# Optimization experiments

Measured on AMD Instinct MI355X. Metric: run time of the kernel, lower is better.

The kernel has to match this reference:

```python
import jax, jax.numpy as jnp
import numpy as np

N_NODES = 100000


def _mean_agg(x, src, dst, n_nodes):
    # gather neighbor (src) features, segment-sum into destination nodes, divide by in-degree
    summed = jax.ops.segment_sum(x[src], dst, num_segments=n_nodes)  # [N, d]
    deg = jax.ops.segment_sum(jnp.ones_like(dst, dtype=x.dtype), dst, num_segments=n_nodes)
    return summed / jnp.clip(deg, 1.0)[:, None]  # DGL clamps zero in-degree to 1


def _sage_conv(x, src, dst, W_self, W_neigh, b, n_nodes):
    h_neigh = _mean_agg(x, src, dst, n_nodes)
    # DGL SAGEConv(mean): fc_self(h_self) + fc_neigh(h_neigh); single bias
    return x @ W_self + h_neigh @ W_neigh + b


def setup_inputs() -> dict:
    key = jax.random.key(0)
    ks = jax.random.split(key, 8)
    in_f, hid_f, out_f = 64, 64, 16
    n_edges = 1200000
    return {
        "x": jax.random.normal(ks[0], (N_NODES, in_f), dtype=jnp.float32),
        "src": jax.random.randint(ks[1], (n_edges,), 0, N_NODES),
        "dst": jax.random.randint(ks[2], (n_edges,), 0, N_NODES),
        "W1_self": jax.random.normal(ks[3], (in_f, hid_f), dtype=jnp.float32) / np.sqrt(in_f),
        "W1_neigh": jax.random.normal(ks[4], (in_f, hid_f), dtype=jnp.float32) / np.sqrt(in_f),
        "b1": jnp.zeros((hid_f,), dtype=jnp.float32),
        "W2_self": jax.random.normal(ks[5], (hid_f, out_f), dtype=jnp.float32) / np.sqrt(hid_f),
        "W2_neigh": jax.random.normal(ks[6], (hid_f, out_f), dtype=jnp.float32) / np.sqrt(hid_f),
        "b2": jnp.zeros((out_f,), dtype=jnp.float32),
    }


def reference(x, src, dst, W1_self, W1_neigh, b1, W2_self, W2_neigh, b2):
    h = _sage_conv(x, src, dst, W1_self, W1_neigh, b1, N_NODES)
    h = jax.nn.relu(h)
    h = _sage_conv(h, src, dst, W2_self, W2_neigh, b2, N_NODES)
    return h
```

## Files before the change

### kernel.cpp

```cpp
#include <hip/hip_runtime.h>

#define N_NODES 100000
#define N_EDGES 1200000
#define BK 64
#define NB 1563
#define CHUNK_E 4096
#define NBLK_E 293
#define TOT_H (NB * NBLK_E)
#define NSB2 ((TOT_H + 1023) / 1024)
#define CAP 1536
#define ND1 3125

#define OFF_ROWPTR 0
#define OFF_HISTG  401408
#define OFF_BLK2   2234368
#define OFF_PAIRS  2236416
#define OFF_SORTED 7036928
#define OFF_Y1     11837440
#define OFF_H1     24637440

__device__ __forceinline__ unsigned short f2bf(float f) {
    unsigned u = __float_as_uint(f);
    unsigned r = (u + 0x7fffu + ((u >> 16) & 1u)) >> 16;
    return (unsigned short)r;
}

__global__ __launch_bounds__(256) void hist_dense1_kernel(
    const int* __restrict__ dst, int* __restrict__ hist_g,
    const float* __restrict__ x,
    const float* __restrict__ Wn, const float* __restrict__ Ws,
    const float* __restrict__ b,
    unsigned short* __restrict__ y1, float* __restrict__ z1)
{
    __shared__ float sx[32 * 64];
    const int t = threadIdx.x;

    if (blockIdx.x < NBLK_E) {
        int* h = (int*)sx;
        const int e0 = blockIdx.x * CHUNK_E;
        const int e1 = min(e0 + CHUNK_E, N_EDGES);
        for (int i = t; i < NB; i += 256) h[i] = 0;
        __syncthreads();
        for (int e = e0 + t; e < e1; e += 256)
            atomicAdd(&h[dst[e] >> 6], 1);
        __syncthreads();
        for (int i = t; i < NB; i += 256)
            hist_g[i * NBLK_E + blockIdx.x] = h[i];
        return;
    }

    const int bid = blockIdx.x - NBLK_E;
    const int w = t >> 6;
    const int lane = t & 63;
    const int half = w >> 1;
    const int nsub = (w & 1) * 16;
    const int chunk = bid * 32;

    {
        const float4* gx = (const float4*)(x + (size_t)chunk * 64);
        float4* sx4 = (float4*)sx;
        sx4[t] = gx[t];
        sx4[t + 256] = gx[t + 256];
    }

    const float* W = half ? Ws : Wn;
    float wr[64];
#pragma unroll
    for (int k = 0; k < 64; ++k) wr[k] = W[k * 64 + lane];
    const float bj = half ? b[lane] : 0.f;

    __syncthreads();

#pragma unroll 2
    for (int m = 0; m < 16; ++m) {
        const int node = nsub + m;
        const float4* xr = (const float4*)(sx + node * 64);
        float a0 = 0.f, a1 = 0.f, a2 = 0.f, a3 = 0.f;
#pragma unroll
        for (int k4 = 0; k4 < 16; ++k4) {
            float4 v = xr[k4];
            a0 += v.x * wr[4 * k4 + 0];
            a1 += v.y * wr[4 * k4 + 1];
            a2 += v.z * wr[4 * k4 + 2];
            a3 += v.w * wr[4 * k4 + 3];
        }
        const float o = (a0 + a1) + (a2 + a3) + bj;
        const size_t gn = (size_t)(chunk + node);
        if (half) z1[gn * 64 + lane] = o;
        else      y1[gn * 64 + lane] = f2bf(o);
    }
}

__global__ __launch_bounds__(1024) void scan2_blocks_kernel(
    int* __restrict__ hist_g, int* __restrict__ blk2)
{
    __shared__ int wsum[16];
    const int t = threadIdx.x;
    const int i = blockIdx.x * 1024 + t;
    const int v = (i < TOT_H) ? hist_g[i] : 0;
    int inc = v;
#pragma unroll
    for (int off = 1; off < 64; off <<= 1) {
        int n = __shfl_up(inc, off);
        if ((t & 63) >= off) inc += n;
    }
    const int wid = t >> 6;
    if ((t & 63) == 63) wsum[wid] = inc;
    __syncthreads();
    if (t < 16) {
        int s = wsum[t];
#pragma unroll
        for (int off = 1; off < 16; off <<= 1) {
            int n = __shfl_up(s, off);
            if (t >= off) s += n;
        }
        wsum[t] = s;
    }
    __syncthreads();
    const int base = (wid > 0) ? wsum[wid - 1] : 0;
    const int incl = inc + base;
    if (i < TOT_H) hist_g[i] = incl - v;
    if (t == 1023) blk2[blockIdx.x] = incl;
}

__global__ __launch_bounds__(512) void tops_scan_kernel(int* __restrict__ blk2)
{
    __shared__ int wsum[8];
    const int t = threadIdx.x;
    const int v = (t < NSB2) ? blk2[t] : 0;
    int inc = v;
#pragma unroll
    for (int off = 1; off < 64; off <<= 1) {
        int n = __shfl_up(inc, off);
        if ((t & 63) >= off) inc += n;
    }
    const int wid = t >> 6;
    if ((t & 63) == 63) wsum[wid] = inc;
    __syncthreads();
    if (t < 8) {
        int s = wsum[t];
#pragma unroll
        for (int off = 1; off < 8; off <<= 1) {
            int n = __shfl_up(s, off);
            if (t >= off) s += n;
        }
        wsum[t] = s;
    }
    __syncthreads();
    const int base = (wid > 0) ? wsum[wid - 1] : 0;
    if (t < NSB2) blk2[t] = inc + base - v;
}

__global__ __launch_bounds__(512) void pair_scatter_kernel(
    const int* __restrict__ src, const int* __restrict__ dst,
    const int* __restrict__ hs_scan, const int* __restrict__ blk2,
    unsigned* __restrict__ pairs)
{
    __shared__ int base_s[NB];
    __shared__ int cur_s[NB];
    const int b = blockIdx.x;
    const int t = threadIdx.x;
    const int e0 = b * CHUNK_E;
    const int e1 = min(e0 + CHUNK_E, N_EDGES);

    for (int i = t; i < NB; i += 512) {
        int idx = i * NBLK_E + b;
        base_s[i] = hs_scan[idx] + blk2[idx >> 10];
        cur_s[i] = 0;
    }
    __syncthreads();
    for (int e = e0 + t; e < e1; e += 512) {
        int d = dst[e];
        int bk = d >> 6;
        int pos = base_s[bk] + atomicAdd(&cur_s[bk], 1);
        pairs[pos] = ((unsigned)src[e] << 6) | (unsigned)(d & 63);
    }
}

__global__ __launch_bounds__(512) void fused_gather1_kernel(
    const unsigned short* __restrict__ y1,
    const unsigned* __restrict__ pairs,
    const int* __restrict__ hs_scan, const int* __restrict__ blk2,
    int* __restrict__ row_ptr, int* __restrict__ sorted_src,
    float* __restrict__ h1)
{
    __shared__ int slist[CAP];
    __shared__ int hist[BK];
    __shared__ int sc[BK];
    __shared__ int cur[BK];
    const int b = blockIdx.x;
    const int t = threadIdx.x;

    const int i0 = b * NBLK_E;
    const int start = hs_scan[i0] + blk2[i0 >> 10];
    const int end = (b == NB - 1) ? N_EDGES
                    : hs_scan[i0 + NBLK_E] + blk2[(i0 + NBLK_E) >> 10];
    const int cnt = end - start;
    const int node0 = b * BK;

    if (t < BK) hist[t] = 0;
    __syncthreads();
    for (int e = start + t; e < end; e += 512)
        atomicAdd(&hist[pairs[e] & 63u], 1);
    __syncthreads();

    int v = 0;
    if (t < BK) {
        v = hist[t];
        int inc = v;
#pragma unroll
        for (int off = 1; off < 64; off <<= 1) {
            int n = __shfl_up(inc, off);
            if (t >= off) inc += n;
        }
        sc[t] = inc;
    }
    __syncthreads();
    const int excl = (t < BK) ? sc[t] - v : 0;
    if (t < BK && node0 + t < N_NODES) row_ptr[node0 + t] = start + excl;
    if (b == NB - 1 && t == 0) row_ptr[N_NODES] = N_EDGES;
    if (t < BK) cur[t] = excl;
    __syncthreads();

    const int wv = t >> 6;
    const int lane = t & 63;
    const int sub = lane >> 5;
    const int sl = lane & 31;
    const int eg = sl >> 3;
    const int fl = sl & 7;

    if (cnt <= CAP) {
        for (int e = start + t; e < end; e += 512) {
            unsigned u = pairs[e];
            int p = atomicAdd(&cur[u & 63u], 1);
            slist[p] = (int)(u >> 6);
        }
        __syncthreads();
        for (int i = t; i < cnt; i += 512)
            sorted_src[start + i] = slist[i];
        for (int q = 0; q < 4; ++q) {
            const int node = wv * 8 + q * 2 + sub;
            const int gn = node0 + node;
            if (gn >= N_NODES) break;
            const int o = sc[node] - hist[node];
            const int dg = hist[node];
            float4* hp = (float4*)(h1 + (size_t)gn * 64);
            float4 z;
            if (eg < 2) z = hp[fl * 2 + eg];
            float a0 = 0.f, a1 = 0.f, a2 = 0.f, a3 = 0.f;
            float a4 = 0.f, a5 = 0.f, a6 = 0.f, a7 = 0.f;
            for (int base = 0; base < dg; base += 8) {
                const int i0e = base + eg;
                const int i1e = base + 4 + eg;
                const bool v0 = i0e < dg, v1 = i1e < dg;
                uint4 r0, r1;
                if (v0) {
                    const int s = slist[o + i0e];
                    r0 = ((const uint4*)(y1 + (size_t)s * 64))[fl];
                }
                if (v1) {
                    const int s = slist[o + i1e];
                    r1 = ((const uint4*)(y1 + (size_t)s * 64))[fl];
                }
                if (v0) {
                    a0 += __uint_as_float(r0.x << 16);
                    a1 += __uint_as_float(r0.x & 0xffff0000u);
                    a2 += __uint_as_float(r0.y << 16);
                    a3 += __uint_as_float(r0.y & 0xffff0000u);
                    a4 += __uint_as_float(r0.z << 16);
                    a5 += __uint_as_float(r0.z & 0xffff0000u);
                    a6 += __uint_as_float(r0.w << 16);
                    a7 += __uint_as_float(r0.w & 0xffff0000u);
                }
                if (v1) {
                    a0 += __uint_as_float(r1.x << 16);
                    a1 += __uint_as_float(r1.x & 0xffff0000u);
                    a2 += __uint_as_float(r1.y << 16);
                    a3 += __uint_as_float(r1.y & 0xffff0000u);
                    a4 += __uint_as_float(r1.z << 16);
                    a5 += __uint_as_float(r1.z & 0xffff0000u);
                    a6 += __uint_as_float(r1.w << 16);
                    a7 += __uint_as_float(r1.w & 0xffff0000u);
                }
            }
#pragma unroll
            for (int d = 8; d <= 16; d <<= 1) {
                a0 += __shfl_xor(a0, d); a1 += __shfl_xor(a1, d);
                a2 += __shfl_xor(a2, d); a3 += __shfl_xor(a3, d);
                a4 += __shfl_xor(a4, d); a5 += __shfl_xor(a5, d);
                a6 += __shfl_xor(a6, d); a7 += __shfl_xor(a7, d);
            }
            const float invd = 1.0f / (float)max(dg, 1);
            if (eg == 0) {
                hp[fl * 2] = make_float4(fmaxf(z.x + a0 * invd, 0.f),
                                         fmaxf(z.y + a1 * invd, 0.f),
                                         fmaxf(z.z + a2 * invd, 0.f),
                                         fmaxf(z.w + a3 * invd, 0.f));
            } else if (eg == 1) {
                hp[fl * 2 + 1] = make_float4(fmaxf(z.x + a4 * invd, 0.f),
                                             fmaxf(z.y + a5 * invd, 0.f),
                                             fmaxf(z.z + a6 * invd, 0.f),
                                             fmaxf(z.w + a7 * invd, 0.f));
            }
        }
    } else {
        if (t < BK) cur[t] = start + excl;
        __syncthreads();
        for (int e = start + t; e < end; e += 512) {
            unsigned u = pairs[e];
            int p = atomicAdd(&cur[u & 63u], 1);
            sorted_src[p] = (int)(u >> 6);
        }
        __syncthreads();
        for (int q = 0; q < 4; ++q) {
            const int node = wv * 8 + q * 2 + sub;
            const int gn = node0 + node;
            if (gn >= N_NODES) break;
            const int o = start + sc[node] - hist[node];
            const int dg = hist[node];
            float4* hp = (float4*)(h1 + (size_t)gn * 64);
            float4 z;
            if (eg < 2) z = hp[fl * 2 + eg];
            float a0 = 0.f, a1 = 0.f, a2 = 0.f, a3 = 0.f;
            float a4 = 0.f, a5 = 0.f, a6 = 0.f, a7 = 0.f;
            for (int base = 0; base < dg; base += 4) {
                const int idx = base + eg;
                if (idx < dg) {
                    const int s = sorted_src[o + idx];
                    uint4 raw = ((const uint4*)(y1 + (size_t)s * 64))[fl];
                    a0 += __uint_as_float(raw.x << 16);
                    a1 += __uint_as_float(raw.x & 0xffff0000u);
                    a2 += __uint_as_float(raw.y << 16);
                    a3 += __uint_as_float(raw.y & 0xffff0000u);
                    a4 += __uint_as_float(raw.z << 16);
                    a5 += __uint_as_float(raw.z & 0xffff0000u);
                    a6 += __uint_as_float(raw.w << 16);
                    a7 += __uint_as_float(raw.w & 0xffff0000u);
                }
            }
#pragma unroll
            for (int d = 8; d <= 16; d <<= 1) {
                a0 += __shfl_xor(a0, d); a1 += __shfl_xor(a1, d);
                a2 += __shfl_xor(a2, d); a3 += __shfl_xor(a3, d);
                a4 += __shfl_xor(a4, d); a5 += __shfl_xor(a5, d);
                a6 += __shfl_xor(a6, d); a7 += __shfl_xor(a7, d);
            }
            const float invd = 1.0f / (float)max(dg, 1);
            if (eg == 0) {
                hp[fl * 2] = make_float4(fmaxf(z.x + a0 * invd, 0.f),
                                         fmaxf(z.y + a1 * invd, 0.f),
                                         fmaxf(z.z + a2 * invd, 0.f),
                                         fmaxf(z.w + a3 * invd, 0.f));
            } else if (eg == 1) {
                hp[fl * 2 + 1] = make_float4(fmaxf(z.x + a4 * invd, 0.f),
                                             fmaxf(z.y + a5 * invd, 0.f),
                                             fmaxf(z.z + a6 * invd, 0.f),
                                             fmaxf(z.w + a7 * invd, 0.f));
            }
        }
    }
}

__global__ __launch_bounds__(256) void dense2_kernel(
    const float* __restrict__ h1,
    const float* __restrict__ Wn, const float* __restrict__ Ws,
    const float* __restrict__ b,
    float* __restrict__ y2, float* __restrict__ out)
{
    __shared__ float sx[32 * 68];
    const int t = threadIdx.x;
    const int w = t >> 6;
    const int lane = t & 63;
    const int half = w >> 1;
    const int nsub = (w & 1) * 16;
    const int j = lane & 15;
    const int g = lane >> 4;
    const int chunk = blockIdx.x * 32;

    {
        const float4* gx = (const float4*)(h1 + (size_t)chunk * 64);
        float4* sx4 = (float4*)sx;
        int r0 = t >> 4, c0 = t & 15;
        sx4[r0 * 17 + c0] = gx[t];
        sx4[(r0 + 16) * 17 + c0] = gx[t + 256];
    }

    const float* W = half ? Ws : Wn;
    float wr[64];
#pragma unroll
    for (int k = 0; k < 64; ++k) wr[k] = W[k * 16 + j];
    const float bj = half ? b[j] : 0.f;

    __syncthreads();

#pragma unroll 2
    for (int q = 0; q < 4; ++q) {
        const int node = nsub + q * 4 + g;
        const float4* xr = (const float4*)(sx + node * 68);
        float a0 = 0.f, a1 = 0.f, a2 = 0.f, a3 = 0.f;
#pragma unroll
        for (int k4 = 0; k4 < 16; ++k4) {
            float4 v = xr[k4];
            a0 += v.x * wr[4 * k4 + 0];
            a1 += v.y * wr[4 * k4 + 1];
            a2 += v.z * wr[4 * k4 + 2];
            a3 += v.w * wr[4 * k4 + 3];
        }
        const float o = (a0 + a1) + (a2 + a3) + bj;
        const size_t gn = (size_t)(chunk + node);
        if (half) out[gn * 16 + j] = o;
        else      y2[gn * 16 + j] = o;
    }
}

__global__ __launch_bounds__(256) void gather2_kernel(
    const float* __restrict__ y2,
    const int* __restrict__ row_ptr,
    const int* __restrict__ sorted_src,
    float* __restrict__ out)
{
    const int wv = threadIdx.x >> 6;
    const int lane = threadIdx.x & 63;
    const int sub = lane >> 4;
    const int sl = lane & 15;
    const int eg = sl >> 2;
    const int fl = sl & 3;

    const int n = blockIdx.x * 16 + wv * 4 + sub;
    const int start = row_ptr[n];
    const int deg = row_ptr[n + 1] - start;

    float4* op = (float4*)(out + (size_t)n * 16);
    float4 z;
    if (eg == 0) z = op[fl];

    float4 acc = make_float4(0.f, 0.f, 0.f, 0.f);
    for (int base = 0; base < deg; base += 16) {
        int eid = 0;
        if (base + sl < deg) eid = sorted_src[start + base + sl];
#pragma unroll
        for (int jj = 0; jj < 16; jj += 4) {
            const int idx = jj + eg;
            const int s = __shfl(eid, sub * 16 + idx);
            if (base + idx < deg) {
                float4 v = ((const float4*)(y2 + (size_t)s * 16))[fl];
                acc.x += v.x; acc.y += v.y; acc.z += v.z; acc.w += v.w;
            }
        }
    }
#pragma unroll
    for (int d = 4; d <= 8; d <<= 1) {
        acc.x += __shfl_xor(acc.x, d); acc.y += __shfl_xor(acc.y, d);
        acc.z += __shfl_xor(acc.z, d); acc.w += __shfl_xor(acc.w, d);
    }
    const float invd = 1.0f / (float)max(deg, 1);
    if (eg == 0) {
        op[fl] = make_float4(z.x + acc.x * invd, z.y + acc.y * invd,
                             z.z + acc.z * invd, z.w + acc.w * invd);
    }
}

extern "C" void kernel_launch(void* const* d_in, const int* in_sizes, int n_in,
                              void* d_out, int out_size, void* d_ws, size_t ws_size,
                              hipStream_t stream) {
    const float* x   = (const float*)d_in[0];
    const int*   src = (const int*)d_in[1];
    const int*   dst = (const int*)d_in[2];
    const float* W1s = (const float*)d_in[3];
    const float* W1n = (const float*)d_in[4];
    const float* b1  = (const float*)d_in[5];
    const float* W2s = (const float*)d_in[6];
    const float* W2n = (const float*)d_in[7];
    const float* b2  = (const float*)d_in[8];
    float* out = (float*)d_out;

    char* ws = (char*)d_ws;
    int* row_ptr    = (int*)(ws + OFF_ROWPTR);
    int* hist_g     = (int*)(ws + OFF_HISTG);
    int* blk2       = (int*)(ws + OFF_BLK2);
    unsigned* pairs = (unsigned*)(ws + OFF_PAIRS);
    int* sorted_src = (int*)(ws + OFF_SORTED);
    unsigned short* y1 = (unsigned short*)(ws + OFF_Y1);
    float* y2       = (float*)(ws + OFF_Y1);
    float* h1       = (float*)(ws + OFF_H1);

    hist_dense1_kernel<<<NBLK_E + ND1, 256, 0, stream>>>(
        dst, hist_g, x, W1n, W1s, b1, y1, h1);
    scan2_blocks_kernel<<<NSB2, 1024, 0, stream>>>(hist_g, blk2);
    tops_scan_kernel<<<1, 512, 0, stream>>>(blk2);
    pair_scatter_kernel<<<NBLK_E, 512, 0, stream>>>(src, dst, hist_g, blk2, pairs);
    fused_gather1_kernel<<<NB, 512, 0, stream>>>(y1, pairs, hist_g, blk2,
                                                 row_ptr, sorted_src, h1);
    dense2_kernel<<<ND1, 256, 0, stream>>>(h1, W2n, W2s, b2, y2, out);
    gather2_kernel<<<N_NODES / 16, 256, 0, stream>>>(y2, row_ptr, sorted_src, out);
}
```

Before: 217.1 us.

## Fuse layer-2 dense projection into layer-1 gather kernel epilogue

The layer-2 projection (h1 times W2_neigh and W2_self plus bias) now runs in the epilogue of the layer-1 gather kernel, using W2 held in shared memory and shuffle reductions, so the separate dense2 kernel is removed. The relu'd h1 row stays in registers instead of being written back and re-read from global memory, and one launch disappears. y2 moves to its own workspace region because y1 is still being read during the fused pass. The cost is more shared memory, more registers and more work per block in the gather kernel, which may lower occupancy.

```diff
diff --git a/kernel.cpp b/kernel.cpp
--- a/kernel.cpp
+++ b/kernel.cpp
@@ -18,6 +18,7 @@
 #define OFF_SORTED 7036928
 #define OFF_Y1     11837440
 #define OFF_H1     24637440
+#define OFF_Y2     50237440
 
 __device__ __forceinline__ unsigned short f2bf(float f) {
     unsigned u = __float_as_uint(f);
@@ -181,15 +182,25 @@
     const unsigned short* __restrict__ y1,
     const unsigned* __restrict__ pairs,
     const int* __restrict__ hs_scan, const int* __restrict__ blk2,
+    const float* __restrict__ h1,
+    const float* __restrict__ W2n, const float* __restrict__ W2s,
+    const float* __restrict__ b2,
     int* __restrict__ row_ptr, int* __restrict__ sorted_src,
-    float* __restrict__ h1)
+    float* __restrict__ y2, float* __restrict__ outp)
 {
     __shared__ int slist[CAP];
     __shared__ int hist[BK];
     __shared__ int sc[BK];
     __shared__ int cur[BK];
+    __shared__ float sW2n[64 * 17];
+    __shared__ float sW2s[64 * 17];
     const int b = blockIdx.x;
     const int t = threadIdx.x;
+
+    for (int e = t; e < 1024; e += 512) {
+        sW2n[(e >> 4) * 17 + (e & 15)] = W2n[e];
+        sW2s[(e >> 4) * 17 + (e & 15)] = W2s[e];
+    }
 
     const int i0 = b * NBLK_E;
     const int start = hs_scan[i0] + blk2[i0 >> 10];
@@ -228,6 +239,7 @@
     const int sl = lane & 31;
     const int eg = sl >> 3;
     const int fl = sl & 7;
+    const float4 bb = ((const float4*)b2)[eg];
 
     if (cnt <= CAP) {
         for (int e = start + t; e < end; e += 512) {
@@ -244,9 +256,9 @@
             if (gn >= N_NODES) break;
             const int o = sc[node] - hist[node];
             const int dg = hist[node];
-            float4* hp = (float4*)(h1 + (size_t)gn * 64);
-            float4 z;
-            if (eg < 2) z = hp[fl * 2 + eg];
+            const float4* hp = (const float4*)(h1 + (size_t)gn * 64);
+            const float4 z0 = hp[fl * 2];
+            const float4 z1v = hp[fl * 2 + 1];
             float a0 = 0.f, a1 = 0.f, a2 = 0.f, a3 = 0.f;
             float a4 = 0.f, a5 = 0.f, a6 = 0.f, a7 = 0.f;
             for (int base = 0; base < dg; base += 8) {
@@ -291,16 +303,41 @@
                 a6 += __shfl_xor(a6, d); a7 += __shfl_xor(a7, d);
             }
             const float invd = 1.0f / (float)max(dg, 1);
-            if (eg == 0) {
-                hp[fl * 2] = make_float4(fmaxf(z.x + a0 * invd, 0.f),
-                                         fmaxf(z.y + a1 * invd, 0.f),
-                                         fmaxf(z.z + a2 * invd, 0.f),
-                                         fmaxf(z.w + a3 * invd, 0.f));
-            } else if (eg == 1) {
-                hp[fl * 2 + 1] = make_float4(fmaxf(z.x + a4 * invd, 0.f),
-                                             fmaxf(z.y + a5 * invd, 0.f),
-                                             fmaxf(z.z + a6 * invd, 0.f),
-                                             fmaxf(z.w + a7 * invd, 0.f));
+            float hv[8];
+            hv[0] = fmaxf(z0.x + a0 * invd, 0.f);
+            hv[1] = fmaxf(z0.y + a1 * invd, 0.f);
+            hv[2] = fmaxf(z0.z + a2 * invd, 0.f);
+            hv[3] = fmaxf(z0.w + a3 * invd, 0.f);
+            hv[4] = fmaxf(z1v.x + a4 * invd, 0.f);
+            hv[5] = fmaxf(z1v.y + a5 * invd, 0.f);
+            hv[6] = fmaxf(z1v.z + a6 * invd, 0.f);
+            hv[7] = fmaxf(z1v.w + a7 * invd, 0.f);
+            float pn0 = 0.f, pn1 = 0.f, pn2 = 0.f, pn3 = 0.f;
+            float ps0 = 0.f, ps1 = 0.f, ps2 = 0.f, ps3 = 0.f;
+            const float* wnB = sW2n + (8 * fl) * 17 + eg * 4;
+            const float* wsB = sW2s + (8 * fl) * 17 + eg * 4;
+#pragma unroll
+            for (int i = 0; i < 8; ++i) {
+                const float h = hv[i];
+                const float* wn = wnB + i * 17;
+                const float* wsp = wsB + i * 17;
+                pn0 += h * wn[0];  pn1 += h * wn[1];
+                pn2 += h * wn[2];  pn3 += h * wn[3];
+                ps0 += h * wsp[0]; ps1 += h * wsp[1];
+                ps2 += h * wsp[2]; ps3 += h * wsp[3];
+            }
+#pragma unroll
+            for (int d = 1; d <= 4; d <<= 1) {
+                pn0 += __shfl_xor(pn0, d); pn1 += __shfl_xor(pn1, d);
+                pn2 += __shfl_xor(pn2, d); pn3 += __shfl_xor(pn3, d);
+                ps0 += __shfl_xor(ps0, d); ps1 += __shfl_xor(ps1, d);
+                ps2 += __shfl_xor(ps2, d); ps3 += __shfl_xor(ps3, d);
+            }
+            if (fl == 0) {
+                ((float4*)(y2 + (size_t)gn * 16))[eg] =
+                    make_float4(pn0, pn1, pn2, pn3);
+                ((float4*)(outp + (size_t)gn * 16))[eg] =
+                    make_float4(ps0 + bb.x, ps1 + bb.y, ps2 + bb.z, ps3 + bb.w);
             }
         }
     } else {
@@ -318,9 +355,9 @@
             if (gn >= N_NODES) break;
             const int o = start + sc[node] - hist[node];
             const int dg = hist[node];
-            float4* hp = (float4*)(h1 + (size_t)gn * 64);
-            float4 z;
-            if (eg < 2) z = hp[fl * 2 + eg];
+            const float4* hp = (const float4*)(h1 + (size_t)gn * 64);
+            const float4 z0 = hp[fl * 2];
+            const float4 z1v = hp[fl * 2 + 1];
             float a0 = 0.f, a1 = 0.f, a2 = 0.f, a3 = 0.f;
             float a4 = 0.f, a5 = 0.f, a6 = 0.f, a7 = 0.f;
             for (int base = 0; base < dg; base += 4) {
@@ -346,70 +383,43 @@
                 a6 += __shfl_xor(a6, d); a7 += __shfl_xor(a7, d);
             }
             const float invd = 1.0f / (float)max(dg, 1);
-            if (eg == 0) {
-                hp[fl * 2] = make_float4(fmaxf(z.x + a0 * invd, 0.f),
-                                         fmaxf(z.y + a1 * invd, 0.f),
-                                         fmaxf(z.z + a2 * invd, 0.f),
-                                         fmaxf(z.w + a3 * invd, 0.f));
-            } else if (eg == 1) {
-                hp[fl * 2 + 1] = make_float4(fmaxf(z.x + a4 * invd, 0.f),
-                                             fmaxf(z.y + a5 * invd, 0.f),
-                                             fmaxf(z.z + a6 * invd, 0.f),
-                                             fmaxf(z.w + a7 * invd, 0.f));
-            }
-        }
-    }
-}
-
-__global__ __launch_bounds__(256) void dense2_kernel(
-    const float* __restrict__ h1,
-    const float* __restrict__ Wn, const float* __restrict__ Ws,
-    const float* __restrict__ b,
-    float* __restrict__ y2, float* __restrict__ out)
-{
-    __shared__ float sx[32 * 68];
-    const int t = threadIdx.x;
-    const int w = t >> 6;
-    const int lane = t & 63;
-    const int half = w >> 1;
-    const int nsub = (w & 1) * 16;
-    const int j = lane & 15;
-    const int g = lane >> 4;
-    const int chunk = blockIdx.x * 32;
-
-    {
-        const float4* gx = (const float4*)(h1 + (size_t)chunk * 64);
-        float4* sx4 = (float4*)sx;
-        int r0 = t >> 4, c0 = t & 15;
-        sx4[r0 * 17 + c0] = gx[t];
-        sx4[(r0 + 16) * 17 + c0] = gx[t + 256];
-    }
-
-    const float* W = half ? Ws : Wn;
-    float wr[64];
-#pragma unroll
-    for (int k = 0; k < 64; ++k) wr[k] = W[k * 16 + j];
-    const float bj = half ? b[j] : 0.f;
-
-    __syncthreads();
-
-#pragma unroll 2
-    for (int q = 0; q < 4; ++q) {
-        const int node = nsub + q * 4 + g;
-        const float4* xr = (const float4*)(sx + node * 68);
-        float a0 = 0.f, a1 = 0.f, a2 = 0.f, a3 = 0.f;
-#pragma unroll
-        for (int k4 = 0; k4 < 16; ++k4) {
-            float4 v = xr[k4];
-            a0 += v.x * wr[4 * k4 + 0];
-            a1 += v.y * wr[4 * k4 + 1];
-            a2 += v.z * wr[4 * k4 + 2];
-            a3 += v.w * wr[4 * k4 + 3];
-        }
-        const float o = (a0 + a1) + (a2 + a3) + bj;
-        const size_t gn = (size_t)(chunk + node);
-        if (half) out[gn * 16 + j] = o;
-        else      y2[gn * 16 + j] = o;
+            float hv[8];
+            hv[0] = fmaxf(z0.x + a0 * invd, 0.f);
+            hv[1] = fmaxf(z0.y + a1 * invd, 0.f);
+            hv[2] = fmaxf(z0.z + a2 * invd, 0.f);
+            hv[3] = fmaxf(z0.w + a3 * invd, 0.f);
+            hv[4] = fmaxf(z1v.x + a4 * invd, 0.f);
+            hv[5] = fmaxf(z1v.y + a5 * invd, 0.f);
+            hv[6] = fmaxf(z1v.z + a6 * invd, 0.f);
+            hv[7] = fmaxf(z1v.w + a7 * invd, 0.f);
+            float pn0 = 0.f, pn1 = 0.f, pn2 = 0.f, pn3 = 0.f;
+            float ps0 = 0.f, ps1 = 0.f, ps2 = 0.f, ps3 = 0.f;
+            const float* wnB = sW2n + (8 * fl) * 17 + eg * 4;
+            const float* wsB = sW2s + (8 * fl) * 17 + eg * 4;
+#pragma unroll
+            for (int i = 0; i < 8; ++i) {
+                const float h = hv[i];
+                const float* wn = wnB + i * 17;
+                const float* wsp = wsB + i * 17;
+                pn0 += h * wn[0];  pn1 += h * wn[1];
+                pn2 += h * wn[2];  pn3 += h * wn[3];
+                ps0 += h * wsp[0]; ps1 += h * wsp[1];
+                ps2 += h * wsp[2]; ps3 += h * wsp[3];
+            }
+#pragma unroll
+            for (int d = 1; d <= 4; d <<= 1) {
+                pn0 += __shfl_xor(pn0, d); pn1 += __shfl_xor(pn1, d);
+                pn2 += __shfl_xor(pn2, d); pn3 += __shfl_xor(pn3, d);
+                ps0 += __shfl_xor(ps0, d); ps1 += __shfl_xor(ps1, d);
+                ps2 += __shfl_xor(ps2, d); ps3 += __shfl_xor(ps3, d);
+            }
+            if (fl == 0) {
+                ((float4*)(y2 + (size_t)gn * 16))[eg] =
+                    make_float4(pn0, pn1, pn2, pn3);
+                ((float4*)(outp + (size_t)gn * 16))[eg] =
+                    make_float4(ps0 + bb.x, ps1 + bb.y, ps2 + bb.z, ps3 + bb.w);
+            }
+        }
     }
 }
 
@@ -481,16 +491,16 @@
     unsigned* pairs = (unsigned*)(ws + OFF_PAIRS);
     int* sorted_src = (int*)(ws + OFF_SORTED);
     unsigned short* y1 = (unsigned short*)(ws + OFF_Y1);
-    float* y2       = (float*)(ws + OFF_Y1);
     float* h1       = (float*)(ws + OFF_H1);
+    float* y2       = (float*)(ws + OFF_Y2);
 
     hist_dense1_kernel<<<NBLK_E + ND1, 256, 0, stream>>>(
         dst, hist_g, x, W1n, W1s, b1, y1, h1);
     scan2_blocks_kernel<<<NSB2, 1024, 0, stream>>>(hist_g, blk2);
     tops_scan_kernel<<<1, 512, 0, stream>>>(blk2);
     pair_scatter_kernel<<<NBLK_E, 512, 0, stream>>>(src, dst, hist_g, blk2, pairs);
-    fused_gather1_kernel<<<NB, 512, 0, stream>>>(y1, pairs, hist_g, blk2,
-                                                 row_ptr, sorted_src, h1);
-    dense2_kernel<<<ND1, 256, 0, stream>>>(h1, W2n, W2s, b2, y2, out);
+    fused_gather1_kernel<<<NB, 512, 0, stream>>>(
+        y1, pairs, hist_g, blk2, h1, W2n, W2s, b2,
+        row_ptr, sorted_src, y2, out);
     gather2_kernel<<<N_NODES / 16, 256, 0, stream>>>(y2, row_ptr, sorted_src, out);
 }
```

New measurement: 230.6 us. 1.06x slower.
